# Optimization experiments

Measured on AMD Instinct MI355X. Metric: run time of the kernel, lower is better.

The kernel has to match this reference:

```python
import jax, jax.numpy as jnp
import numpy as np

B, C, H, W = 32, 2, 512, 512


def setup_inputs() -> dict:
    key = jax.random.key(0)
    k1, k2 = jax.random.split(key)
    inp = jax.random.normal(k1, (B, C, H, W), dtype=jnp.float32)
    tgt = jax.random.normal(k2, (B, C, H, W), dtype=jnp.float32)
    return {"input": inp, "target": tgt}


def reference(input, target):
    b, c, h, w = input.shape
    dt = input.dtype
    # coordinate maps: (index+1)/size, kept fused via broadcasting
    x_map = jnp.arange(1, w + 1, dtype=dt) / w          # [W]
    y_map = (jnp.arange(1, h + 1, dtype=dt) / h)[:, None]  # [H,1]
    # per-(sample, channel) softmax over flattened heatmap (DSNT)
    sm = jax.nn.softmax(input.reshape(b, c, h * w), axis=-1).reshape(b, c, h, w)
    # soft-argmax coords in normalized range, then *size -> pixel coords
    pred_x = jnp.sum(sm * x_map, axis=(-2, -1)) * w     # [B,C] pixel
    pred_y = jnp.sum(sm * y_map, axis=(-2, -1)) * h     # [B,C] pixel
    # hard argmax for ground truth; ((idx % W + 1)/W)*W == idx % W + 1
    idx = jnp.argmax(target.reshape(b, c, h * w), axis=-1)  # [B,C]
    true_x = (idx % w + 1).astype(dt)                   # [B,C] pixel
    true_y = (idx // w + 1).astype(dt)                  # [B,C] pixel
    # per-point euclidean pixel distance
    ed = jnp.sqrt((true_x - pred_x) ** 2 + (true_y - pred_y) ** 2)  # [B,C]
    s_i = jnp.sum(ed[:, 0])  # channel 0: inferior
    s_s = jnp.sum(ed[:, 1])  # channel 1: superior
    # diameter (distance between the two points) difference, abs via sqrt(sq)
    pred_pts = jnp.stack([pred_x, pred_y], axis=-1)  # [B,C,2]
    true_pts = jnp.stack([true_x, true_y], axis=-1)  # [B,C,2]
    vp = pred_pts[:, 0] - pred_pts[:, 1]             # [B,2]
    vt = true_pts[:, 0] - true_pts[:, 1]             # [B,2]
    pred_dist = jnp.sqrt(jnp.sum(vp ** 2, axis=-1))
    true_dist = jnp.sqrt(jnp.sum(vt ** 2, axis=-1))
    s_diam = jnp.sum(jnp.sqrt((pred_dist - true_dist) ** 2))
    bn = jnp.asarray(b, dt)
    # coordinate lists (pixel coord - 1 as index), ordered batch-major then channel
    pred_coords = (pred_pts - 1.0).reshape(b * c, 2)
    true_coords = (true_pts - 1.0).reshape(b * c, 2)
    return (s_i / bn, s_s / bn, (s_i + s_s) / bn, s_diam / bn,
            pred_coords, true_coords)
```

## Files before the change

kernel.cpp:

```cpp
#include <hip/hip_runtime.h>
#include <math.h>

#define BATCH 32
#define CHANS 2
#define HH 512
#define WW 512
#define BC (BATCH * CHANS)
#define HMAP (HH * WW)
#define SPLITS 64
#define CHUNK (HMAP / SPLITS)
#define THREADS 256

__device__ __forceinline__ void async_ld16_nt(const float* g, float* lds) {
    __builtin_amdgcn_global_load_lds(
        (const __attribute__((address_space(1))) void*)g,
        (__attribute__((address_space(3))) void*)lds,
        16, 0, 2);
}

__global__ __launch_bounds__(THREADS)
void dsnt_partial(const float* __restrict__ inp, const float* __restrict__ tgt,
                  float* __restrict__ ps, float* __restrict__ psx,
                  float* __restrict__ psy, float* __restrict__ pmv,
                  int* __restrict__ pix) {
    __shared__ float s_in[CHUNK];
    __shared__ float s_tg[CHUNK];

    const int split = blockIdx.x;
    const int bc    = blockIdx.y;
    const long base = (long)bc * HMAP + (long)split * CHUNK;
    const int t    = threadIdx.x;
    const int lane = t & 63;
    const int wave = t >> 6;

    const int wbase = wave * 1024;
    #pragma unroll
    for (int j = 0; j < 4; ++j)
        async_ld16_nt(inp + base + wbase + j * 256 + lane * 4,
                      &s_in[wbase + j * 256]);
    #pragma unroll
    for (int j = 0; j < 4; ++j)
        async_ld16_nt(tgt + base + wbase + j * 256 + lane * 4,
                      &s_tg[wbase + j * 256]);

    __builtin_amdgcn_s_waitcnt(0);
    __syncthreads();

    float s = 0.f, sx = 0.f, sy = 0.f;
    float bm = -INFINITY;
    int   bi = 0;

    const float4* s_in4 = (const float4*)s_in;
    const float4* s_tg4 = (const float4*)s_tg;

    #pragma unroll
    for (int j = 0; j < 4; ++j) {
        const int fi = wave * 256 + j * 64 + lane;
        const int p  = split * CHUNK + fi * 4;
        const float4 x = s_in4[fi];
        const float4 g = s_tg4[fi];
        const float wy = (float)((p >> 9) + 1);
        const float wx = (float)((p & 511) + 1);
        const float e0 = __expf(x.x), e1 = __expf(x.y);
        const float e2 = __expf(x.z), e3 = __expf(x.w);
        const float es = (e0 + e1) + (e2 + e3);
        s  += es;
        sx += es * wx + (e1 + 2.f * e2 + 3.f * e3);
        sy += es * wy;
        if (g.x > bm) { bm = g.x; bi = p;     }
        if (g.y > bm) { bm = g.y; bi = p + 1; }
        if (g.z > bm) { bm = g.z; bi = p + 2; }
        if (g.w > bm) { bm = g.w; bi = p + 3; }
    }

    #pragma unroll
    for (int off = 32; off > 0; off >>= 1) {
        s  += __shfl_down(s,  off, 64);
        sx += __shfl_down(sx, off, 64);
        sy += __shfl_down(sy, off, 64);
        const float om = __shfl_down(bm, off, 64);
        const int   oi = __shfl_down(bi, off, 64);
        if (om > bm || (om == bm && oi < bi)) { bm = om; bi = oi; }
    }

    __shared__ float shs[4], shsx[4], shsy[4], shm[4];
    __shared__ int   shi[4];
    if (lane == 0) { shs[wave] = s; shsx[wave] = sx; shsy[wave] = sy;
                     shm[wave] = bm; shi[wave] = bi; }
    __syncthreads();
    if (t == 0) {
        float S = shs[0], SX = shsx[0], SY = shsy[0], M = shm[0];
        int   I = shi[0];
        #pragma unroll
        for (int w = 1; w < 4; ++w) {
            S += shs[w]; SX += shsx[w]; SY += shsy[w];
            if (shm[w] > M || (shm[w] == M && shi[w] < I)) { M = shm[w]; I = shi[w]; }
        }
        const int o = split * BC + bc;
        ps[o] = S; psx[o] = SX; psy[o] = SY; pmv[o] = M; pix[o] = I;
    }
}

__global__ __launch_bounds__(256)
void dsnt_final(const float* __restrict__ ps, const float* __restrict__ psx,
                const float* __restrict__ psy, const float* __restrict__ pmv,
                const int* __restrict__ pix, float* __restrict__ out) {
    const int t    = threadIdx.x;
    const int lane = t & 63;
    const int wv   = t >> 6;

    float S = 0.f, SX = 0.f, SY = 0.f, M = -INFINITY;
    int I = 0;
    #pragma unroll
    for (int k = 0; k < SPLITS / 4; ++k) {
        const int o = (wv * (SPLITS / 4) + k) * BC + lane;
        S += ps[o]; SX += psx[o]; SY += psy[o];
        const float v = pmv[o];
        const int  ix = pix[o];
        if (v > M || (v == M && ix < I)) { M = v; I = ix; }
    }

    __shared__ float lS[4][64], lSX[4][64], lSY[4][64], lM[4][64];
    __shared__ int   lI[4][64];
    lS[wv][lane] = S; lSX[wv][lane] = SX; lSY[wv][lane] = SY;
    lM[wv][lane] = M; lI[wv][lane] = I;
    __syncthreads();
    if (wv != 0) return;

    #pragma unroll
    for (int w = 1; w < 4; ++w) {
        S += lS[w][lane]; SX += lSX[w][lane]; SY += lSY[w][lane];
        const float v = lM[w][lane];
        const int  ix = lI[w][lane];
        if (v > M || (v == M && ix < I)) { M = v; I = ix; }
    }

    const float px = SX / S;
    const float py = SY / S;
    const float tx = (float)((I & 511) + 1);
    const float ty = (float)((I >> 9) + 1);
    const float dx = tx - px, dy = ty - py;
    const float ed = sqrtf(dx * dx + dy * dy);

    out[4 + lane * 2 + 0]   = px - 1.f;
    out[4 + lane * 2 + 1]   = py - 1.f;
    out[132 + lane * 2 + 0] = tx - 1.f;
    out[133 + lane * 2]     = ty - 1.f;

    const float opx = __shfl_xor(px, 1, 64);
    const float opy = __shfl_xor(py, 1, 64);
    const float otx = __shfl_xor(tx, 1, 64);
    const float oty = __shfl_xor(ty, 1, 64);
    float dterm = 0.f;
    if ((lane & 1) == 0) {
        const float vpx = px - opx, vpy = py - opy;
        const float vtx = tx - otx, vty = ty - oty;
        const float pd = sqrtf(vpx * vpx + vpy * vpy);
        const float td = sqrtf(vtx * vtx + vty * vty);
        dterm = fabsf(pd - td);
    }
    float e0 = ((lane & 1) == 0) ? ed : 0.f;
    float e1 = ((lane & 1) == 1) ? ed : 0.f;
    #pragma unroll
    for (int off = 32; off > 0; off >>= 1) {
        e0    += __shfl_down(e0, off, 64);
        e1    += __shfl_down(e1, off, 64);
        dterm += __shfl_down(dterm, off, 64);
    }
    if (lane == 0) {
        const float inv = 1.0f / (float)BATCH;
        out[0] = e0 * inv;
        out[1] = e1 * inv;
        out[2] = (e0 + e1) * inv;
        out[3] = dterm * inv;
    }
}

extern "C" void kernel_launch(void* const* d_in, const int* in_sizes, int n_in,
                              void* d_out, int out_size, void* d_ws, size_t ws_size,
                              hipStream_t stream) {
    const float* inp = (const float*)d_in[0];
    const float* tgt = (const float*)d_in[1];
    float* out = (float*)d_out;

    float* ps  = (float*)d_ws;
    float* psx = ps  + BC * SPLITS;
    float* psy = psx + BC * SPLITS;
    float* pmv = psy + BC * SPLITS;
    int*   pix = (int*)(pmv + BC * SPLITS);

    dim3 grid(SPLITS, BC);
    dsnt_partial<<<grid, THREADS, 0, stream>>>(inp, tgt, ps, psx, psy, pmv, pix);
    dsnt_final<<<1, 256, 0, stream>>>(ps, psx, psy, pmv, pix, out);
}
```

Baseline: 143.7 us.

## Double-buffer per-wave async LDS loads over larger chunks with fewer blocks

Cuts the partial-reduction grid from 64 splits per heatmap to 8. Each wave now walks a private 8192-float region in 1024-float sub-chunks, double-buffered in LDS, so direct-to-LDS global loads for the next sub-chunk overlap the exp and argmax work on the current one. The aim is to hide memory latency within each wave and to reduce block launch and partial-result overhead. The trade-off is fewer blocks (512) for the whole GPU and hand-written vmcnt/lgkmcnt waits that must match the load count exactly.

```diff
diff --git a/kernel.cpp b/kernel.cpp
--- a/kernel.cpp
+++ b/kernel.cpp
@@ -7,9 +7,12 @@
 #define WW 512
 #define BC (BATCH * CHANS)
 #define HMAP (HH * WW)
-#define SPLITS 64
+#define SPLITS 8
 #define CHUNK (HMAP / SPLITS)
 #define THREADS 256
+#define WAVE_FLOATS 8192
+#define SUB 1024
+#define NSUB (WAVE_FLOATS / SUB)
 
 __device__ __forceinline__ void async_ld16_nt(const float* g, float* lds) {
     __builtin_amdgcn_global_load_lds(
@@ -18,60 +21,77 @@
         16, 0, 2);
 }
 
+#define WAITV8 asm volatile("s_waitcnt vmcnt(8)" ::: "memory")
+#define WAITV0 asm volatile("s_waitcnt vmcnt(0)" ::: "memory")
+#define WAITL0 asm volatile("s_waitcnt lgkmcnt(0)" ::: "memory")
+
 __global__ __launch_bounds__(THREADS)
 void dsnt_partial(const float* __restrict__ inp, const float* __restrict__ tgt,
                   float* __restrict__ ps, float* __restrict__ psx,
                   float* __restrict__ psy, float* __restrict__ pmv,
                   int* __restrict__ pix) {
-    __shared__ float s_in[CHUNK];
-    __shared__ float s_tg[CHUNK];
+    __shared__ float s_in[4][2][SUB];
+    __shared__ float s_tg[4][2][SUB];
 
     const int split = blockIdx.x;
     const int bc    = blockIdx.y;
-    const long base = (long)bc * HMAP + (long)split * CHUNK;
-    const int t    = threadIdx.x;
-    const int lane = t & 63;
-    const int wave = t >> 6;
-
-    const int wbase = wave * 1024;
-    #pragma unroll
-    for (int j = 0; j < 4; ++j)
-        async_ld16_nt(inp + base + wbase + j * 256 + lane * 4,
-                      &s_in[wbase + j * 256]);
-    #pragma unroll
-    for (int j = 0; j < 4; ++j)
-        async_ld16_nt(tgt + base + wbase + j * 256 + lane * 4,
-                      &s_tg[wbase + j * 256]);
-
-    __builtin_amdgcn_s_waitcnt(0);
-    __syncthreads();
+    const int t     = threadIdx.x;
+    const int lane  = t & 63;
+    const int wave  = t >> 6;
+    const long base = (long)bc * HMAP + (long)split * CHUNK
+                    + (long)wave * WAVE_FLOATS;
+    const float* gin = inp + base;
+    const float* gtg = tgt + base;
+    const int pbase = split * CHUNK + wave * WAVE_FLOATS;
 
     float s = 0.f, sx = 0.f, sy = 0.f;
     float bm = -INFINITY;
     int   bi = 0;
 
-    const float4* s_in4 = (const float4*)s_in;
-    const float4* s_tg4 = (const float4*)s_tg;
-
-    #pragma unroll
-    for (int j = 0; j < 4; ++j) {
-        const int fi = wave * 256 + j * 64 + lane;
-        const int p  = split * CHUNK + fi * 4;
-        const float4 x = s_in4[fi];
-        const float4 g = s_tg4[fi];
-        const float wy = (float)((p >> 9) + 1);
-        const float wx = (float)((p & 511) + 1);
-        const float e0 = __expf(x.x), e1 = __expf(x.y);
-        const float e2 = __expf(x.z), e3 = __expf(x.w);
-        const float es = (e0 + e1) + (e2 + e3);
-        s  += es;
-        sx += es * wx + (e1 + 2.f * e2 + 3.f * e3);
-        sy += es * wy;
-        if (g.x > bm) { bm = g.x; bi = p;     }
-        if (g.y > bm) { bm = g.y; bi = p + 1; }
-        if (g.z > bm) { bm = g.z; bi = p + 2; }
-        if (g.w > bm) { bm = g.w; bi = p + 3; }
-    }
+    auto fill = [&](int buf, int k) {
+        #pragma unroll
+        for (int j = 0; j < 4; ++j)
+            async_ld16_nt(gin + k * SUB + j * 256 + lane * 4,
+                          &s_in[wave][buf][j * 256]);
+        #pragma unroll
+        for (int j = 0; j < 4; ++j)
+            async_ld16_nt(gtg + k * SUB + j * 256 + lane * 4,
+                          &s_tg[wave][buf][j * 256]);
+    };
+
+    auto consume = [&](int buf, int k) {
+        const float4* bin = (const float4*)&s_in[wave][buf][0];
+        const float4* btg = (const float4*)&s_tg[wave][buf][0];
+        #pragma unroll
+        for (int j = 0; j < 4; ++j) {
+            const int fi = j * 64 + lane;
+            const int p  = pbase + k * SUB + fi * 4;
+            const float4 x = bin[fi];
+            const float4 g = btg[fi];
+            const float wy = (float)((p >> 9) + 1);
+            const float wx = (float)((p & 511) + 1);
+            const float e0 = __expf(x.x), e1 = __expf(x.y);
+            const float e2 = __expf(x.z), e3 = __expf(x.w);
+            const float es = (e0 + e1) + (e2 + e3);
+            s  += es;
+            sx += es * wx + (e1 + 2.f * e2 + 3.f * e3);
+            sy += es * wy;
+            if (g.x > bm) { bm = g.x; bi = p;     }
+            if (g.y > bm) { bm = g.y; bi = p + 1; }
+            if (g.z > bm) { bm = g.z; bi = p + 2; }
+            if (g.w > bm) { bm = g.w; bi = p + 3; }
+        }
+    };
+
+    fill(0, 0); fill(1, 1);
+    WAITV8; consume(0, 0); WAITL0; fill(0, 2);
+    WAITV8; consume(1, 1); WAITL0; fill(1, 3);
+    WAITV8; consume(0, 2); WAITL0; fill(0, 4);
+    WAITV8; consume(1, 3); WAITL0; fill(1, 5);
+    WAITV8; consume(0, 4); WAITL0; fill(0, 6);
+    WAITV8; consume(1, 5); WAITL0; fill(1, 7);
+    WAITV8; consume(0, 6);
+    WAITV0; consume(1, 7);
 
     #pragma unroll
     for (int off = 32; off > 0; off >>= 1) {
```

Measured after the change: 140.4 us. 1.02x faster.
